# Kernel tuning notes

Measured on AMD Instinct MI355X. Metric: run time of the kernel, lower is better.

Reference implementation:

```python
import jax, jax.numpy as jnp
import numpy as np

B, F, S, D = 256, 8, 200, 64
H = 36  # hidden units per field
EPS = 1e-3  # Dice BN epsilon


def setup_inputs() -> dict:
    key0 = jax.random.key(0)
    ks = jax.random.split(key0, 8)
    query = jax.random.normal(ks[0], (B, F, D), dtype=jnp.float32)
    key = jax.random.normal(ks[1], (B, F, S, D), dtype=jnp.float32)
    sequence_num = jax.random.randint(ks[2], (B, F), 1, S + 1, dtype=jnp.int32)
    W_h = jax.random.normal(ks[3], (F, 3 * D, H), dtype=jnp.float32) * 0.05
    b_h = jnp.zeros((F, H), dtype=jnp.float32)
    alpha = jnp.zeros((F,), dtype=jnp.float32)
    W_o = jax.random.normal(ks[4], (F, H, 1), dtype=jnp.float32) * 0.05
    b_o = jnp.zeros((F, 1), dtype=jnp.float32)
    return {"query": query, "key": key, "W_h": W_h, "b_h": b_h,
            "alpha": alpha, "W_o": W_o, "b_o": b_o,
            "sequence_num": sequence_num, "training": 1}


def reference(query, key, W_h, b_h, alpha, W_o, b_o, sequence_num, training):
    # query: [B,F,D], key: [B,F,S,D]
    q = query[:, :, None, :]                      # broadcast instead of tile
    qb = jnp.broadcast_to(q, key.shape)           # [B,F,S,D]
    cat = jnp.concatenate([key, qb, q - key], axis=-1)  # [B,F,S,3D]
    # per-field Dense(36), vectorized across fields
    h = jnp.einsum('bfsc,fch->bfsh', cat, W_h) + b_h[None, :, None, :]
    # Dice: BatchNorm (no affine, training-mode batch stats over batch+seq per field/feature)
    mean = h.mean(axis=(0, 2), keepdims=True)
    var = h.var(axis=(0, 2), keepdims=True)
    p = jax.nn.sigmoid((h - mean) * jax.lax.rsqrt(var + EPS))
    h = (alpha[None, :, None, None] * (1.0 - p) + p) * h
    # per-field Dense(1) -> attention scores [B,F,S]
    scores = jnp.einsum('bfsh,fh->bfs', h, W_o[:, :, 0]) + b_o[None, :, 0, None]
    # mask invalid positions and softmax over sequence
    mask = jnp.arange(key.shape[2])[None, None, :] < sequence_num[:, :, None]
    scores = jnp.where(mask, scores, -jnp.inf)
    attn = jax.nn.softmax(scores, axis=-1)        # [B,F,S]
    # weighted sum over sequence -> [B,F,D]
    return jnp.einsum('bfs,bfsd->bfd', attn, key)
```

## Files before the change

kernel.cpp:

```cpp
#include <hip/hip_runtime.h>
#include <math.h>

#define NB 256
#define NF 8
#define NS 200
#define ND 64
#define NH 36
#define MT 13
#define EPSV 1e-3f

#define WS_SUM 0
#define WS_SQ  288
#define WS_QT  1152
#define WS_WK  (1152 + 2048 * 48)

typedef __attribute__((ext_vector_type(8))) short short8;
typedef __attribute__((ext_vector_type(4))) float f32x4;

__device__ __forceinline__ unsigned short f32_to_bf16(float x) {
    unsigned u = __float_as_uint(x);
    unsigned r = u + 0x7FFFu + ((u >> 16) & 1u);
    return (unsigned short)(r >> 16);
}
__device__ __forceinline__ float bf16_to_f32(unsigned short h) {
    return __uint_as_float(((unsigned)h) << 16);
}
__device__ __forceinline__ short8 cvt8(float4 a, float4 b) {
    short8 r;
    r[0] = (short)f32_to_bf16(a.x); r[1] = (short)f32_to_bf16(a.y);
    r[2] = (short)f32_to_bf16(a.z); r[3] = (short)f32_to_bf16(a.w);
    r[4] = (short)f32_to_bf16(b.x); r[5] = (short)f32_to_bf16(b.y);
    r[6] = (short)f32_to_bf16(b.z); r[7] = (short)f32_to_bf16(b.w);
    return r;
}

__global__ __launch_bounds__(256) void k_prep(
    const float* __restrict__ query, const float* __restrict__ W_h,
    const float* __restrict__ b_h, float* __restrict__ ws)
{
    const int blk = blockIdx.x, tid = threadIdx.x;
    if (blk < NF) {
        const int f = blk;
        const float* Wf = W_h + (size_t)f * (3 * ND * NH);
        unsigned short* wk = (unsigned short*)(ws + WS_WK) + f * (48 * ND);
        for (int i = tid; i < 48 * ND; i += 256) {
            int h = i >> 6, d = i & 63;
            float v = (h < NH) ? (Wf[d * NH + h] - Wf[(2 * ND + d) * NH + h]) : 0.f;
            wk[h * ND + d] = f32_to_bf16(v);
        }
    } else if (blk == NF) {
        for (int i = tid; i < 576; i += 256) ws[i] = 0.f;
    } else {
        const int b = blk - NF - 1;
        __shared__ float qs[NF * ND];
        for (int i = tid; i < NF * ND; i += 256)
            qs[i] = query[(size_t)b * NF * ND + i];
        __syncthreads();
        for (int i = tid; i < NF * 48; i += 256) {
            int f = i / 48, h = i - f * 48;
            float acc = 0.f;
            if (h < NH) {
                const float* Wf = W_h + (size_t)f * (3 * ND * NH);
                acc = b_h[f * NH + h];
                for (int d = 0; d < ND; ++d)
                    acc += qs[f * ND + d] * (Wf[(ND + d) * NH + h] + Wf[(2 * ND + d) * NH + h]);
            }
            ws[WS_QT + (size_t)(b * NF + f) * 48 + h] = acc;
        }
    }
}

__global__ __launch_bounds__(256, 3) void k_stats(
    const float* __restrict__ key, float* __restrict__ ws)
{
    const int blk = blockIdx.x;
    const int f = blk & (NF - 1);
    const int tid = threadIdx.x;
    const int lane = tid & 63;
    const int wv = tid >> 6;
    const int col = lane & 15;
    const int quad = lane >> 4;

    __shared__ float sumP[48], sqP[48];
    if (tid < 48) { sumP[tid] = 0.f; sqP[tid] = 0.f; }
    __syncthreads();

    const float* kbase = key + (size_t)blk * (NS * ND);
    const unsigned short* wk = (const unsigned short*)(ws + WS_WK) + f * (48 * ND);

    float4 pf[4][4];
    #pragma unroll
    for (int t = 0; t < 4; ++t) {
        const int mt = wv + 4 * t;
        if (mt < MT) {
            const int s = 16 * mt + col;
            const float4* p = (const float4*)(kbase + (size_t)(s < NS ? s : NS - 1) * ND + quad * 8);
            pf[t][0] = p[0]; pf[t][1] = p[1];
            pf[t][2] = p[8]; pf[t][3] = p[9];
        }
    }

    short8 bfr[3][2];
    float qv[3];
    #pragma unroll
    for (int nt = 0; nt < 3; ++nt) {
        #pragma unroll
        for (int ks = 0; ks < 2; ++ks)
            bfr[nt][ks] = *(const short8*)&wk[(nt * 16 + col) * ND + ks * 32 + quad * 8];
        qv[nt] = ws[WS_QT + (size_t)blk * 48 + nt * 16 + col];
    }

    float s_sum[3] = {0.f, 0.f, 0.f}, s_sq[3] = {0.f, 0.f, 0.f};
    #pragma unroll
    for (int t = 0; t < 4; ++t) {
        const int mt = wv + 4 * t;
        if (mt < MT) {
            short8 ah0 = cvt8(pf[t][0], pf[t][1]);
            short8 ah1 = cvt8(pf[t][2], pf[t][3]);
            #pragma unroll
            for (int nt = 0; nt < 3; ++nt) {
                f32x4 acc = {qv[nt], qv[nt], qv[nt], qv[nt]};
                acc = __builtin_amdgcn_mfma_f32_16x16x32_bf16(ah0, bfr[nt][0], acc, 0, 0, 0);
                acc = __builtin_amdgcn_mfma_f32_16x16x32_bf16(ah1, bfr[nt][1], acc, 0, 0, 0);
                #pragma unroll
                for (int r = 0; r < 4; ++r) {
                    int srow = 16 * mt + quad * 4 + r;
                    if (srow < NS) { float v = acc[r]; s_sum[nt] += v; s_sq[nt] += v * v; }
                }
            }
        }
    }
    #pragma unroll
    for (int nt = 0; nt < 3; ++nt) {
        float sv = s_sum[nt], qq = s_sq[nt];
        sv += __shfl_xor(sv, 16, 64); sv += __shfl_xor(sv, 32, 64);
        qq += __shfl_xor(qq, 16, 64); qq += __shfl_xor(qq, 32, 64);
        if (quad == 0) {
            atomicAdd(&sumP[nt * 16 + col], sv);
            atomicAdd(&sqP[nt * 16 + col], qq);
        }
    }
    __syncthreads();
    if (tid < NH) {
        atomicAdd(&ws[WS_SUM + f * NH + tid], sumP[tid]);
        atomicAdd(&ws[WS_SQ + f * NH + tid], sqP[tid]);
    }
}

__global__ __launch_bounds__(256, 3) void k_attn(
    const float* __restrict__ key, const float* __restrict__ alpha,
    const float* __restrict__ W_o, const float* __restrict__ b_o,
    const int* __restrict__ seqn, const float* __restrict__ ws,
    float* __restrict__ out)
{
    const int blk = blockIdx.x;
    const int f = blk & (NF - 1);
    const int tid = threadIdx.x;
    const int lane = tid & 63;
    const int wv = tid >> 6;
    const int col = lane & 15;
    const int quad = lane >> 4;

    __shared__ float sw[208];
    __shared__ float redM[4], redS[4];
    __shared__ float pout[4][64];

    const float* kbase = key + (size_t)blk * (NS * ND);
    const unsigned short* wk = (const unsigned short*)(ws + WS_WK) + f * (48 * ND);
    const float inv_n = 1.f / (float)(NB * NS);

    short8 kah[4][2];
    {
        float4 pf[4][4];
        const float4 z4 = {0.f, 0.f, 0.f, 0.f};
        pf[3][0] = z4; pf[3][1] = z4; pf[3][2] = z4; pf[3][3] = z4;
        #pragma unroll
        for (int t = 0; t < 4; ++t) {
            const int mt = wv + 4 * t;
            if (mt < MT) {
                const int s = 16 * mt + col;
                const float4* p = (const float4*)(kbase + (size_t)(s < NS ? s : NS - 1) * ND + quad * 8);
                pf[t][0] = p[0]; pf[t][1] = p[1];
                pf[t][2] = p[8]; pf[t][3] = p[9];
            }
        }
        #pragma unroll
        for (int t = 0; t < 4; ++t) {
            kah[t][0] = cvt8(pf[t][0], pf[t][1]);
            kah[t][1] = cvt8(pf[t][2], pf[t][3]);
        }
    }

    short8 bfr[3][2];
    float qv[3], mn[3], iv[3], wo[3];
    #pragma unroll
    for (int nt = 0; nt < 3; ++nt) {
        #pragma unroll
        for (int ks = 0; ks < 2; ++ks)
            bfr[nt][ks] = *(const short8*)&wk[(nt * 16 + col) * ND + ks * 32 + quad * 8];
        const int hh = nt * 16 + col;
        const bool hv = hh < NH;
        const int hc = hv ? hh : 0;
        qv[nt] = ws[WS_QT + (size_t)blk * 48 + hh];
        const float sm = ws[WS_SUM + f * NH + hc];
        const float sq = ws[WS_SQ + f * NH + hc];
        const float m = sm * inv_n;
        mn[nt] = m;
        iv[nt] = rsqrtf(fmaxf(sq * inv_n - m * m, 0.f) + EPSV);
        wo[nt] = hv ? W_o[f * NH + hh] : 0.f;
    }
    const float alf = alpha[f];
    const float bo = b_o[f];
    const int sq_n = seqn[blk];

    #pragma unroll
    for (int t = 0; t < 4; ++t) {
        const int mt = wv + 4 * t;
        if (mt < MT) {
            float part[4] = {0.f, 0.f, 0.f, 0.f};
            #pragma unroll
            for (int nt = 0; nt < 3; ++nt) {
                f32x4 acc = {qv[nt], qv[nt], qv[nt], qv[nt]};
                acc = __builtin_amdgcn_mfma_f32_16x16x32_bf16(kah[t][0], bfr[nt][0], acc, 0, 0, 0);
                acc = __builtin_amdgcn_mfma_f32_16x16x32_bf16(kah[t][1], bfr[nt][1], acc, 0, 0, 0);
                #pragma unroll
                for (int r = 0; r < 4; ++r) {
                    const float h = acc[r];
                    const float pg = 1.f / (1.f + __expf(-(h - mn[nt]) * iv[nt]));
                    part[r] += (alf + (1.f - alf) * pg) * h * wo[nt];
                }
            }
            #pragma unroll
            for (int r = 0; r < 4; ++r) {
                float v = part[r];
                v += __shfl_xor(v, 1, 64);
                v += __shfl_xor(v, 2, 64);
                v += __shfl_xor(v, 4, 64);
                v += __shfl_xor(v, 8, 64);
                const int srow = 16 * mt + quad * 4 + r;
                if (col == 0 && srow < NS) sw[srow] = v + bo;
            }
        }
    }
    __syncthreads();

    const bool valid = (tid < 208) && (tid < sq_n);
    const float sc = valid ? sw[tid] : -1e30f;
    float m = sc;
    m = fmaxf(m, __shfl_xor(m, 1, 64));  m = fmaxf(m, __shfl_xor(m, 2, 64));
    m = fmaxf(m, __shfl_xor(m, 4, 64));  m = fmaxf(m, __shfl_xor(m, 8, 64));
    m = fmaxf(m, __shfl_xor(m, 16, 64)); m = fmaxf(m, __shfl_xor(m, 32, 64));
    if (lane == 0) redM[wv] = m;
    __syncthreads();
    const float maxv = fmaxf(fmaxf(redM[0], redM[1]), fmaxf(redM[2], redM[3]));
    const float e = valid ? __expf(sc - maxv) : 0.f;
    float l = e;
    l += __shfl_xor(l, 1, 64);  l += __shfl_xor(l, 2, 64);
    l += __shfl_xor(l, 4, 64);  l += __shfl_xor(l, 8, 64);
    l += __shfl_xor(l, 16, 64); l += __shfl_xor(l, 32, 64);
    if (lane == 0) redS[wv] = l;
    __syncthreads();
    const float isum = 1.f / (redS[0] + redS[1] + redS[2] + redS[3]);
    if (tid < 208) sw[tid] = e * isum;
    __syncthreads();

    float po0[8] = {0,0,0,0,0,0,0,0}, po1[8] = {0,0,0,0,0,0,0,0};
    #pragma unroll
    for (int t = 0; t < 4; ++t) {
        const int mt = wv + 4 * t;
        if (mt < MT) {
            const float w = sw[16 * mt + col];
            #pragma unroll
            for (int j = 0; j < 8; ++j) {
                po0[j] += w * bf16_to_f32((unsigned short)kah[t][0][j]);
                po1[j] += w * bf16_to_f32((unsigned short)kah[t][1][j]);
            }
        }
    }
    #pragma unroll
    for (int off = 1; off <= 8; off <<= 1) {
        #pragma unroll
        for (int j = 0; j < 8; ++j) {
            po0[j] += __shfl_xor(po0[j], off, 64);
            po1[j] += __shfl_xor(po1[j], off, 64);
        }
    }
    if (col == 0) {
        #pragma unroll
        for (int j = 0; j < 8; ++j) {
            pout[wv][quad * 8 + j] = po0[j];
            pout[wv][32 + quad * 8 + j] = po1[j];
        }
    }
    __syncthreads();
    if (tid < 64)
        out[(size_t)blk * ND + tid] =
            pout[0][tid] + pout[1][tid] + pout[2][tid] + pout[3][tid];
}

extern "C" void kernel_launch(void* const* d_in, const int* in_sizes, int n_in,
                              void* d_out, int out_size, void* d_ws, size_t ws_size,
                              hipStream_t stream) {
    const float* query = (const float*)d_in[0];
    const float* key   = (const float*)d_in[1];
    const float* W_h   = (const float*)d_in[2];
    const float* b_h   = (const float*)d_in[3];
    const float* alpha = (const float*)d_in[4];
    const float* W_o   = (const float*)d_in[5];
    const float* b_o   = (const float*)d_in[6];
    const int*   seqn  = (const int*)d_in[7];
    float* out = (float*)d_out;
    float* ws  = (float*)d_ws;

    k_prep<<<NB + NF + 1, 256, 0, stream>>>(query, W_h, b_h, ws);
    k_stats<<<NB * NF, 256, 0, stream>>>(key, ws);
    k_attn<<<NB * NF, 256, 0, stream>>>(key, alpha, W_o, b_o, seqn, ws, out);
}
```

Measured before the change: 210.7 us.

## Cache bf16-converted key tiles in workspace and spread stat atomics across copies

k_stats now writes its bf16-converted key fragments, already in MFMA register layout, to a workspace buffer. k_attn reads that half-size copy instead of re-reading and re-converting the fp32 key. The batch-norm sum and sum-of-squares atomics are split across 8 replicated accumulators to reduce contention, and k_attn sums the 8 copies into shared memory before use. k_attn's occupancy hint rises from 3 to 4 blocks per SM. In exchange, k_stats gains an extra global write, so total DRAM traffic may stay about the same unless the bf16 copy stays resident in the large last-level cache.

```diff
diff --git a/kernel.cpp b/kernel.cpp
--- a/kernel.cpp
+++ b/kernel.cpp
@@ -8,11 +8,13 @@
 #define NH 36
 #define MT 13
 #define EPSV 1e-3f
+#define NCPY 8
 
 #define WS_SUM 0
-#define WS_SQ  288
-#define WS_QT  1152
-#define WS_WK  (1152 + 2048 * 48)
+#define WS_SQ  (NCPY * 288)
+#define WS_QT  (2 * NCPY * 288)
+#define WS_WK  (WS_QT + 2048 * 48)
+#define WS_KC  (WS_WK + (NF * 48 * ND) / 2)
 
 typedef __attribute__((ext_vector_type(8))) short short8;
 typedef __attribute__((ext_vector_type(4))) float f32x4;
@@ -49,7 +51,7 @@
             wk[h * ND + d] = f32_to_bf16(v);
         }
     } else if (blk == NF) {
-        for (int i = tid; i < 576; i += 256) ws[i] = 0.f;
+        for (int i = tid; i < 2 * NCPY * 288; i += 256) ws[i] = 0.f;
     } else {
         const int b = blk - NF - 1;
         __shared__ float qs[NF * ND];
@@ -87,6 +89,7 @@
 
     const float* kbase = key + (size_t)blk * (NS * ND);
     const unsigned short* wk = (const unsigned short*)(ws + WS_WK) + f * (48 * ND);
+    unsigned short* kc = (unsigned short*)(ws + WS_KC);
 
     float4 pf[4][4];
     #pragma unroll
@@ -117,6 +120,9 @@
         if (mt < MT) {
             short8 ah0 = cvt8(pf[t][0], pf[t][1]);
             short8 ah1 = cvt8(pf[t][2], pf[t][3]);
+            const size_t cb = ((size_t)(blk * MT + mt) * 64 + lane) * 16;
+            *(short8*)&kc[cb] = ah0;
+            *(short8*)&kc[cb + 8] = ah1;
             #pragma unroll
             for (int nt = 0; nt < 3; ++nt) {
                 f32x4 acc = {qv[nt], qv[nt], qv[nt], qv[nt]};
@@ -142,13 +148,14 @@
     }
     __syncthreads();
     if (tid < NH) {
-        atomicAdd(&ws[WS_SUM + f * NH + tid], sumP[tid]);
-        atomicAdd(&ws[WS_SQ + f * NH + tid], sqP[tid]);
-    }
-}
-
-__global__ __launch_bounds__(256, 3) void k_attn(
-    const float* __restrict__ key, const float* __restrict__ alpha,
+        const int c = (blk >> 3) & (NCPY - 1);
+        atomicAdd(&ws[WS_SUM + c * 288 + f * NH + tid], sumP[tid]);
+        atomicAdd(&ws[WS_SQ  + c * 288 + f * NH + tid], sqP[tid]);
+    }
+}
+
+__global__ __launch_bounds__(256, 4) void k_attn(
+    const float* __restrict__ alpha,
     const float* __restrict__ W_o, const float* __restrict__ b_o,
     const int* __restrict__ seqn, const float* __restrict__ ws,
     float* __restrict__ out)
@@ -164,32 +171,35 @@
     __shared__ float sw[208];
     __shared__ float redM[4], redS[4];
     __shared__ float pout[4][64];
-
-    const float* kbase = key + (size_t)blk * (NS * ND);
+    __shared__ float ssum[NH], ssq[NH];
+
     const unsigned short* wk = (const unsigned short*)(ws + WS_WK) + f * (48 * ND);
+    const unsigned short* kc = (const unsigned short*)(ws + WS_KC);
     const float inv_n = 1.f / (float)(NB * NS);
 
+    if (tid < NH) {
+        float a = 0.f, b2 = 0.f;
+        #pragma unroll
+        for (int c = 0; c < NCPY; ++c) {
+            a  += ws[WS_SUM + c * 288 + f * NH + tid];
+            b2 += ws[WS_SQ  + c * 288 + f * NH + tid];
+        }
+        ssum[tid] = a; ssq[tid] = b2;
+    }
+
     short8 kah[4][2];
-    {
-        float4 pf[4][4];
-        const float4 z4 = {0.f, 0.f, 0.f, 0.f};
-        pf[3][0] = z4; pf[3][1] = z4; pf[3][2] = z4; pf[3][3] = z4;
-        #pragma unroll
-        for (int t = 0; t < 4; ++t) {
-            const int mt = wv + 4 * t;
-            if (mt < MT) {
-                const int s = 16 * mt + col;
-                const float4* p = (const float4*)(kbase + (size_t)(s < NS ? s : NS - 1) * ND + quad * 8);
-                pf[t][0] = p[0]; pf[t][1] = p[1];
-                pf[t][2] = p[8]; pf[t][3] = p[9];
-            }
-        }
-        #pragma unroll
-        for (int t = 0; t < 4; ++t) {
-            kah[t][0] = cvt8(pf[t][0], pf[t][1]);
-            kah[t][1] = cvt8(pf[t][2], pf[t][3]);
-        }
-    }
+    kah[3][0] = short8{0,0,0,0,0,0,0,0};
+    kah[3][1] = short8{0,0,0,0,0,0,0,0};
+    #pragma unroll
+    for (int t = 0; t < 4; ++t) {
+        const int mt = wv + 4 * t;
+        if (mt < MT) {
+            const size_t cb = ((size_t)(blk * MT + mt) * 64 + lane) * 16;
+            kah[t][0] = *(const short8*)&kc[cb];
+            kah[t][1] = *(const short8*)&kc[cb + 8];
+        }
+    }
+    __syncthreads();
 
     short8 bfr[3][2];
     float qv[3], mn[3], iv[3], wo[3];
@@ -202,8 +212,8 @@
         const bool hv = hh < NH;
         const int hc = hv ? hh : 0;
         qv[nt] = ws[WS_QT + (size_t)blk * 48 + hh];
-        const float sm = ws[WS_SUM + f * NH + hc];
-        const float sq = ws[WS_SQ + f * NH + hc];
+        const float sm = ssum[hc];
+        const float sq = ssq[hc];
         const float m = sm * inv_n;
         mn[nt] = m;
         iv[nt] = rsqrtf(fmaxf(sq * inv_n - m * m, 0.f) + EPSV);
@@ -314,5 +324,5 @@
 
     k_prep<<<NB + NF + 1, 256, 0, stream>>>(query, W_h, b_h, ws);
     k_stats<<<NB * NF, 256, 0, stream>>>(key, ws);
-    k_attn<<<NB * NF, 256, 0, stream>>>(key, alpha, W_o, b_o, seqn, ws, out);
-}
+    k_attn<<<NB * NF, 256, 0, stream>>>(alpha, W_o, b_o, seqn, ws, out);
+}
```

Result: no change. 212.8 us (+1.0%).

## Replace global atomic BN stats with per-block partials reduced in attention kernel

Applied to the files above, without the earlier changes.

Each k_stats block now writes its per-field sum and sum-of-squares partials to a dedicated workspace slot instead of doing global atomicAdds into shared counters. That removes the zeroing block from k_prep and the atomic contention on 72 addresses. Every k_attn block then re-reduces the 256 partials for its field, overlapping that reduction with its key loads. This adds redundant reduction work and extra workspace reads per block, and k_stats launch bounds are raised to 4 blocks per SM.

```diff
diff --git a/kernel.cpp b/kernel.cpp
--- a/kernel.cpp
+++ b/kernel.cpp
@@ -9,10 +9,9 @@
 #define MT 13
 #define EPSV 1e-3f
 
-#define WS_SUM 0
-#define WS_SQ  288
-#define WS_QT  1152
-#define WS_WK  (1152 + 2048 * 48)
+#define WS_QT   0
+#define WS_WK   (2048 * 48)
+#define WS_PART (WS_WK + 12288)
 
 typedef __attribute__((ext_vector_type(8))) short short8;
 typedef __attribute__((ext_vector_type(4))) float f32x4;
@@ -48,10 +47,8 @@
             float v = (h < NH) ? (Wf[d * NH + h] - Wf[(2 * ND + d) * NH + h]) : 0.f;
             wk[h * ND + d] = f32_to_bf16(v);
         }
-    } else if (blk == NF) {
-        for (int i = tid; i < 576; i += 256) ws[i] = 0.f;
     } else {
-        const int b = blk - NF - 1;
+        const int b = blk - NF;
         __shared__ float qs[NF * ND];
         for (int i = tid; i < NF * ND; i += 256)
             qs[i] = query[(size_t)b * NF * ND + i];
@@ -70,11 +67,12 @@
     }
 }
 
-__global__ __launch_bounds__(256, 3) void k_stats(
+__global__ __launch_bounds__(256, 4) void k_stats(
     const float* __restrict__ key, float* __restrict__ ws)
 {
     const int blk = blockIdx.x;
     const int f = blk & (NF - 1);
+    const int b = blk >> 3;
     const int tid = threadIdx.x;
     const int lane = tid & 63;
     const int wv = tid >> 6;
@@ -86,9 +84,12 @@
     __syncthreads();
 
     const float* kbase = key + (size_t)blk * (NS * ND);
-    const unsigned short* wk = (const unsigned short*)(ws + WS_WK) + f * (48 * ND);
 
     float4 pf[4][4];
+    {
+        const float4 z4 = {0.f, 0.f, 0.f, 0.f};
+        pf[3][0] = z4; pf[3][1] = z4; pf[3][2] = z4; pf[3][3] = z4;
+    }
     #pragma unroll
     for (int t = 0; t < 4; ++t) {
         const int mt = wv + 4 * t;
@@ -100,13 +101,14 @@
         }
     }
 
+    const unsigned short* wkg = (const unsigned short*)(ws + WS_WK) + f * (48 * ND);
     short8 bfr[3][2];
     float qv[3];
     #pragma unroll
     for (int nt = 0; nt < 3; ++nt) {
         #pragma unroll
         for (int ks = 0; ks < 2; ++ks)
-            bfr[nt][ks] = *(const short8*)&wk[(nt * 16 + col) * ND + ks * 32 + quad * 8];
+            bfr[nt][ks] = *(const short8*)&wkg[(nt * 16 + col) * ND + ks * 32 + quad * 8];
         qv[nt] = ws[WS_QT + (size_t)blk * 48 + nt * 16 + col];
     }
 
@@ -142,8 +144,9 @@
     }
     __syncthreads();
     if (tid < NH) {
-        atomicAdd(&ws[WS_SUM + f * NH + tid], sumP[tid]);
-        atomicAdd(&ws[WS_SQ + f * NH + tid], sqP[tid]);
+        float* P = ws + WS_PART + ((size_t)f * NB + b) * 72;
+        P[tid] = sumP[tid];
+        P[36 + tid] = sqP[tid];
     }
 }
 
@@ -164,46 +167,65 @@
     __shared__ float sw[208];
     __shared__ float redM[4], redS[4];
     __shared__ float pout[4][64];
+    __shared__ float red2[2][72];
+    __shared__ float ssum[NH], ssq[NH];
 
     const float* kbase = key + (size_t)blk * (NS * ND);
-    const unsigned short* wk = (const unsigned short*)(ws + WS_WK) + f * (48 * ND);
     const float inv_n = 1.f / (float)(NB * NS);
 
-    short8 kah[4][2];
+    float4 pf[4][4];
     {
-        float4 pf[4][4];
         const float4 z4 = {0.f, 0.f, 0.f, 0.f};
         pf[3][0] = z4; pf[3][1] = z4; pf[3][2] = z4; pf[3][3] = z4;
-        #pragma unroll
-        for (int t = 0; t < 4; ++t) {
-            const int mt = wv + 4 * t;
-            if (mt < MT) {
-                const int s = 16 * mt + col;
-                const float4* p = (const float4*)(kbase + (size_t)(s < NS ? s : NS - 1) * ND + quad * 8);
-                pf[t][0] = p[0]; pf[t][1] = p[1];
-                pf[t][2] = p[8]; pf[t][3] = p[9];
-            }
-        }
-        #pragma unroll
-        for (int t = 0; t < 4; ++t) {
-            kah[t][0] = cvt8(pf[t][0], pf[t][1]);
-            kah[t][1] = cvt8(pf[t][2], pf[t][3]);
-        }
-    }
-
+    }
+    #pragma unroll
+    for (int t = 0; t < 4; ++t) {
+        const int mt = wv + 4 * t;
+        if (mt < MT) {
+            const int s = 16 * mt + col;
+            const float4* p = (const float4*)(kbase + (size_t)(s < NS ? s : NS - 1) * ND + quad * 8);
+            pf[t][0] = p[0]; pf[t][1] = p[1];
+            pf[t][2] = p[8]; pf[t][3] = p[9];
+        }
+    }
+
+    if (tid < 144) {
+        const int j = tid % 72, half = tid / 72;
+        const float* P = ws + WS_PART + (size_t)f * NB * 72;
+        float a = 0.f;
+        #pragma unroll 8
+        for (int bb = half * 128; bb < half * 128 + 128; ++bb)
+            a += P[(size_t)bb * 72 + j];
+        red2[half][j] = a;
+    }
+    __syncthreads();
+    if (tid < NH) {
+        ssum[tid] = red2[0][tid] + red2[1][tid];
+        ssq[tid]  = red2[0][36 + tid] + red2[1][36 + tid];
+    }
+
+    short8 kah[4][2];
+    #pragma unroll
+    for (int t = 0; t < 4; ++t) {
+        kah[t][0] = cvt8(pf[t][0], pf[t][1]);
+        kah[t][1] = cvt8(pf[t][2], pf[t][3]);
+    }
+    __syncthreads();
+
+    const unsigned short* wkg = (const unsigned short*)(ws + WS_WK) + f * (48 * ND);
     short8 bfr[3][2];
     float qv[3], mn[3], iv[3], wo[3];
     #pragma unroll
     for (int nt = 0; nt < 3; ++nt) {
         #pragma unroll
         for (int ks = 0; ks < 2; ++ks)
-            bfr[nt][ks] = *(const short8*)&wk[(nt * 16 + col) * ND + ks * 32 + quad * 8];
+            bfr[nt][ks] = *(const short8*)&wkg[(nt * 16 + col) * ND + ks * 32 + quad * 8];
         const int hh = nt * 16 + col;
         const bool hv = hh < NH;
         const int hc = hv ? hh : 0;
         qv[nt] = ws[WS_QT + (size_t)blk * 48 + hh];
-        const float sm = ws[WS_SUM + f * NH + hc];
-        const float sq = ws[WS_SQ + f * NH + hc];
+        const float sm = ssum[hc];
+        const float sq = ssq[hc];
         const float m = sm * inv_n;
         mn[nt] = m;
         iv[nt] = rsqrtf(fmaxf(sq * inv_n - m * m, 0.f) + EPSV);
@@ -312,7 +334,7 @@
     float* out = (float*)d_out;
     float* ws  = (float*)d_ws;
 
-    k_prep<<<NB + NF + 1, 256, 0, stream>>>(query, W_h, b_h, ws);
+    k_prep<<<NB + NF, 256, 0, stream>>>(query, W_h, b_h, ws);
     k_stats<<<NB * NF, 256, 0, stream>>>(key, ws);
     k_attn<<<NB * NF, 256, 0, stream>>>(key, alpha, W_o, b_o, seqn, ws, out);
 }
```

After: 225.1 us. 1.07x slower.

## Fuse stats and attention into a cooperative kernel keeping key tiles in registers

Applied to the files above, without the earlier changes.

Replaces the separate stats and attention kernels with a single cooperative grid of 512 blocks. Each block processes four (b,f) rows, keeps their bf16-converted key tiles in registers across a grid-wide sync, then computes the Dice attention and weighted sum without re-reading key from global memory. This halves key traffic and removes one launch. The cost is heavy register pressure (launch bounds lowered to 2 blocks per CU), lower parallelism, and a grid-sync wait; if the cooperative launch fails, it falls back to the old two-kernel path.

```diff
diff --git a/kernel.cpp b/kernel.cpp
--- a/kernel.cpp
+++ b/kernel.cpp
@@ -1,5 +1,8 @@
 #include <hip/hip_runtime.h>
+#include <hip/hip_cooperative_groups.h>
 #include <math.h>
+
+namespace cg = cooperative_groups;
 
 #define NB 256
 #define NF 8
@@ -8,6 +11,8 @@
 #define NH 36
 #define MT 13
 #define EPSV 1e-3f
+#define NBLK 512
+#define NTILE 4
 
 #define WS_SUM 0
 #define WS_SQ  288
@@ -70,7 +75,212 @@
     }
 }
 
-__global__ __launch_bounds__(256, 3) void k_stats(
+__global__ __launch_bounds__(256, 2) void k_main(
+    const float* __restrict__ key, const float* __restrict__ alpha,
+    const float* __restrict__ W_o, const float* __restrict__ b_o,
+    const int* __restrict__ seqn, float* __restrict__ ws,
+    float* __restrict__ out)
+{
+    const int blk = blockIdx.x;
+    const int f = blk & (NF - 1);
+    const int tid = threadIdx.x;
+    const int lane = tid & 63;
+    const int wv = tid >> 6;
+    const int col = lane & 15;
+    const int quad = lane >> 4;
+
+    __shared__ float sumP[48], sqP[48];
+    __shared__ float sw[208];
+    __shared__ float redM[4], redS[4];
+    __shared__ float pout[4][64];
+
+    if (tid < 48) { sumP[tid] = 0.f; sqP[tid] = 0.f; }
+    __syncthreads();
+
+    const unsigned short* wkg = (const unsigned short*)(ws + WS_WK) + f * (48 * ND);
+    short8 bfr[3][2];
+    #pragma unroll
+    for (int nt = 0; nt < 3; ++nt)
+        #pragma unroll
+        for (int ks = 0; ks < 2; ++ks)
+            bfr[nt][ks] = *(const short8*)&wkg[(nt * 16 + col) * ND + ks * 32 + quad * 8];
+
+    short8 kah[NTILE][4][2];
+    float qv[NTILE][3];
+    float s_sum[3] = {0.f, 0.f, 0.f}, s_sq[3] = {0.f, 0.f, 0.f};
+
+    #pragma unroll
+    for (int tile = 0; tile < NTILE; ++tile) {
+        const int tb = blk + tile * NBLK;
+        const float* kbase = key + (size_t)tb * (NS * ND);
+        #pragma unroll
+        for (int nt = 0; nt < 3; ++nt)
+            qv[tile][nt] = ws[WS_QT + (size_t)tb * 48 + nt * 16 + col];
+
+        float4 pf[4][4];
+        {
+            const float4 z4 = {0.f, 0.f, 0.f, 0.f};
+            pf[3][0] = z4; pf[3][1] = z4; pf[3][2] = z4; pf[3][3] = z4;
+        }
+        #pragma unroll
+        for (int t = 0; t < 4; ++t) {
+            const int mt = wv + 4 * t;
+            if (mt < MT) {
+                const int s = 16 * mt + col;
+                const float4* p = (const float4*)(kbase + (size_t)(s < NS ? s : NS - 1) * ND + quad * 8);
+                pf[t][0] = p[0]; pf[t][1] = p[1];
+                pf[t][2] = p[8]; pf[t][3] = p[9];
+            }
+        }
+        #pragma unroll
+        for (int t = 0; t < 4; ++t) {
+            const int mt = wv + 4 * t;
+            short8 a0 = cvt8(pf[t][0], pf[t][1]);
+            short8 a1 = cvt8(pf[t][2], pf[t][3]);
+            kah[tile][t][0] = a0;
+            kah[tile][t][1] = a1;
+            if (mt < MT) {
+                #pragma unroll
+                for (int nt = 0; nt < 3; ++nt) {
+                    f32x4 acc = {qv[tile][nt], qv[tile][nt], qv[tile][nt], qv[tile][nt]};
+                    acc = __builtin_amdgcn_mfma_f32_16x16x32_bf16(a0, bfr[nt][0], acc, 0, 0, 0);
+                    acc = __builtin_amdgcn_mfma_f32_16x16x32_bf16(a1, bfr[nt][1], acc, 0, 0, 0);
+                    #pragma unroll
+                    for (int r = 0; r < 4; ++r) {
+                        int srow = 16 * mt + quad * 4 + r;
+                        if (srow < NS) { float v = acc[r]; s_sum[nt] += v; s_sq[nt] += v * v; }
+                    }
+                }
+            }
+        }
+    }
+    #pragma unroll
+    for (int nt = 0; nt < 3; ++nt) {
+        float sv = s_sum[nt], qq = s_sq[nt];
+        sv += __shfl_xor(sv, 16, 64); sv += __shfl_xor(sv, 32, 64);
+        qq += __shfl_xor(qq, 16, 64); qq += __shfl_xor(qq, 32, 64);
+        if (quad == 0) {
+            atomicAdd(&sumP[nt * 16 + col], sv);
+            atomicAdd(&sqP[nt * 16 + col], qq);
+        }
+    }
+    __syncthreads();
+    if (tid < NH) {
+        atomicAdd(&ws[WS_SUM + f * NH + tid], sumP[tid]);
+        atomicAdd(&ws[WS_SQ + f * NH + tid], sqP[tid]);
+    }
+
+    cg::this_grid().sync();
+
+    const float inv_n = 1.f / (float)(NB * NS);
+    float mn[3], iv[3], wo[3];
+    #pragma unroll
+    for (int nt = 0; nt < 3; ++nt) {
+        const int hh = nt * 16 + col;
+        const bool hv = hh < NH;
+        const int hc = hv ? hh : 0;
+        const float sm = ws[WS_SUM + f * NH + hc];
+        const float sq = ws[WS_SQ + f * NH + hc];
+        const float m = sm * inv_n;
+        mn[nt] = m;
+        iv[nt] = rsqrtf(fmaxf(sq * inv_n - m * m, 0.f) + EPSV);
+        wo[nt] = hv ? W_o[f * NH + hh] : 0.f;
+    }
+    const float alf = alpha[f];
+    const float bo = b_o[f];
+
+    for (int tile = 0; tile < NTILE; ++tile) {
+        const int tb = blk + tile * NBLK;
+        const int sq_n = seqn[tb];
+
+        #pragma unroll
+        for (int t = 0; t < 4; ++t) {
+            const int mt = wv + 4 * t;
+            if (mt < MT) {
+                float part[4] = {0.f, 0.f, 0.f, 0.f};
+                #pragma unroll
+                for (int nt = 0; nt < 3; ++nt) {
+                    f32x4 acc = {qv[tile][nt], qv[tile][nt], qv[tile][nt], qv[tile][nt]};
+                    acc = __builtin_amdgcn_mfma_f32_16x16x32_bf16(kah[tile][t][0], bfr[nt][0], acc, 0, 0, 0);
+                    acc = __builtin_amdgcn_mfma_f32_16x16x32_bf16(kah[tile][t][1], bfr[nt][1], acc, 0, 0, 0);
+                    #pragma unroll
+                    for (int r = 0; r < 4; ++r) {
+                        const float h = acc[r];
+                        const float pg = 1.f / (1.f + __expf(-(h - mn[nt]) * iv[nt]));
+                        part[r] += (alf + (1.f - alf) * pg) * h * wo[nt];
+                    }
+                }
+                #pragma unroll
+                for (int r = 0; r < 4; ++r) {
+                    float v = part[r];
+                    v += __shfl_xor(v, 1, 64);
+                    v += __shfl_xor(v, 2, 64);
+                    v += __shfl_xor(v, 4, 64);
+                    v += __shfl_xor(v, 8, 64);
+                    const int srow = 16 * mt + quad * 4 + r;
+                    if (col == 0 && srow < NS) sw[srow] = v + bo;
+                }
+            }
+        }
+        __syncthreads();
+
+        const bool valid = (tid < 208) && (tid < sq_n);
+        const float sc = valid ? sw[tid] : -1e30f;
+        float m = sc;
+        m = fmaxf(m, __shfl_xor(m, 1, 64));  m = fmaxf(m, __shfl_xor(m, 2, 64));
+        m = fmaxf(m, __shfl_xor(m, 4, 64));  m = fmaxf(m, __shfl_xor(m, 8, 64));
+        m = fmaxf(m, __shfl_xor(m, 16, 64)); m = fmaxf(m, __shfl_xor(m, 32, 64));
+        if (lane == 0) redM[wv] = m;
+        __syncthreads();
+        const float maxv = fmaxf(fmaxf(redM[0], redM[1]), fmaxf(redM[2], redM[3]));
+        const float e = valid ? __expf(sc - maxv) : 0.f;
+        float l = e;
+        l += __shfl_xor(l, 1, 64);  l += __shfl_xor(l, 2, 64);
+        l += __shfl_xor(l, 4, 64);  l += __shfl_xor(l, 8, 64);
+        l += __shfl_xor(l, 16, 64); l += __shfl_xor(l, 32, 64);
+        if (lane == 0) redS[wv] = l;
+        __syncthreads();
+        const float isum = 1.f / (redS[0] + redS[1] + redS[2] + redS[3]);
+        if (tid < 208) sw[tid] = e * isum;
+        __syncthreads();
+
+        float po0[8] = {0,0,0,0,0,0,0,0}, po1[8] = {0,0,0,0,0,0,0,0};
+        #pragma unroll
+        for (int t = 0; t < 4; ++t) {
+            const int mt = wv + 4 * t;
+            if (mt < MT) {
+                const float w = sw[16 * mt + col];
+                #pragma unroll
+                for (int j = 0; j < 8; ++j) {
+                    po0[j] += w * bf16_to_f32((unsigned short)kah[tile][t][0][j]);
+                    po1[j] += w * bf16_to_f32((unsigned short)kah[tile][t][1][j]);
+                }
+            }
+        }
+        #pragma unroll
+        for (int off = 1; off <= 8; off <<= 1) {
+            #pragma unroll
+            for (int j = 0; j < 8; ++j) {
+                po0[j] += __shfl_xor(po0[j], off, 64);
+                po1[j] += __shfl_xor(po1[j], off, 64);
+            }
+        }
+        if (col == 0) {
+            #pragma unroll
+            for (int j = 0; j < 8; ++j) {
+                pout[wv][quad * 8 + j] = po0[j];
+                pout[wv][32 + quad * 8 + j] = po1[j];
+            }
+        }
+        __syncthreads();
+        if (tid < 64)
+            out[(size_t)tb * ND + tid] =
+                pout[0][tid] + pout[1][tid] + pout[2][tid] + pout[3][tid];
+        __syncthreads();
+    }
+}
+
+__global__ __launch_bounds__(256, 3) void k_stats_fb(
     const float* __restrict__ key, float* __restrict__ ws)
 {
     const int blk = blockIdx.x;
@@ -86,9 +296,13 @@
     __syncthreads();
 
     const float* kbase = key + (size_t)blk * (NS * ND);
-    const unsigned short* wk = (const unsigned short*)(ws + WS_WK) + f * (48 * ND);
+    const unsigned short* wkg = (const unsigned short*)(ws + WS_WK) + f * (48 * ND);
 
     float4 pf[4][4];
+    {
+        const float4 z4 = {0.f, 0.f, 0.f, 0.f};
+        pf[3][0] = z4; pf[3][1] = z4; pf[3][2] = z4; pf[3][3] = z4;
+    }
     #pragma unroll
     for (int t = 0; t < 4; ++t) {
         const int mt = wv + 4 * t;
@@ -106,7 +320,7 @@
     for (int nt = 0; nt < 3; ++nt) {
         #pragma unroll
         for (int ks = 0; ks < 2; ++ks)
-            bfr[nt][ks] = *(const short8*)&wk[(nt * 16 + col) * ND + ks * 32 + quad * 8];
+            bfr[nt][ks] = *(const short8*)&wkg[(nt * 16 + col) * ND + ks * 32 + quad * 8];
         qv[nt] = ws[WS_QT + (size_t)blk * 48 + nt * 16 + col];
     }
 
@@ -147,7 +361,7 @@
     }
 }
 
-__global__ __launch_bounds__(256, 3) void k_attn(
+__global__ __launch_bounds__(256, 3) void k_attn_fb(
     const float* __restrict__ key, const float* __restrict__ alpha,
     const float* __restrict__ W_o, const float* __restrict__ b_o,
     const int* __restrict__ seqn, const float* __restrict__ ws,
@@ -166,7 +380,7 @@
     __shared__ float pout[4][64];
 
     const float* kbase = key + (size_t)blk * (NS * ND);
-    const unsigned short* wk = (const unsigned short*)(ws + WS_WK) + f * (48 * ND);
+    const unsigned short* wkg = (const unsigned short*)(ws + WS_WK) + f * (48 * ND);
     const float inv_n = 1.f / (float)(NB * NS);
 
     short8 kah[4][2];
@@ -197,7 +411,7 @@
     for (int nt = 0; nt < 3; ++nt) {
         #pragma unroll
         for (int ks = 0; ks < 2; ++ks)
-            bfr[nt][ks] = *(const short8*)&wk[(nt * 16 + col) * ND + ks * 32 + quad * 8];
+            bfr[nt][ks] = *(const short8*)&wkg[(nt * 16 + col) * ND + ks * 32 + quad * 8];
         const int hh = nt * 16 + col;
         const bool hv = hh < NH;
         const int hc = hv ? hh : 0;
@@ -313,6 +527,14 @@
     float* ws  = (float*)d_ws;
 
     k_prep<<<NB + NF + 1, 256, 0, stream>>>(query, W_h, b_h, ws);
-    k_stats<<<NB * NF, 256, 0, stream>>>(key, ws);
-    k_attn<<<NB * NF, 256, 0, stream>>>(key, alpha, W_o, b_o, seqn, ws, out);
-}
+
+    void* args[] = {(void*)&key, (void*)&alpha, (void*)&W_o, (void*)&b_o,
+                    (void*)&seqn, (void*)&ws, (void*)&out};
+    hipError_t ce = hipLaunchCooperativeKernel((const void*)k_main, dim3(NBLK),
+                                               dim3(256), args, 0, stream);
+    if (ce != hipSuccess) {
+        (void)hipGetLastError();
+        k_stats_fb<<<NB * NF, 256, 0, stream>>>(key, ws);
+        k_attn_fb<<<NB * NF, 256, 0, stream>>>(key, alpha, W_o, b_o, seqn, ws, out);
+    }
+}
```

Result: slower. 308.1 us (+46.2%).
